# Kernel tuning notes

Hardware: AMD Instinct MI355X
Metric: run time of the kernel (lower is better)

Reference implementation:

```python
import jax
jax.config.update("jax_enable_x64", True)
import jax.numpy as jnp
import numpy as np

SAMPLE_RATE = 44100
HOP = 512
B, N_MELS, T = 8, 128, 2048
L = T * HOP  # 1,048,576 samples


def _lerp_up(x, out_len):
    # torch F.interpolate(mode='linear', align_corners=True): [B,C,Tin]->[B,C,out_len]
    t_in = x.shape[-1]
    pos = jnp.arange(out_len, dtype=jnp.float64) * ((t_in - 1) / (out_len - 1))
    i0 = jnp.floor(pos).astype(jnp.int32)
    i1 = jnp.minimum(i0 + 1, t_in - 1)
    w = (pos - i0).astype(x.dtype)
    return x[..., i0] * (1 - w) + x[..., i1] * w


def _conv1d(x, w, b, pad):
    y = jax.lax.conv_general_dilated(x, w, (1,), [(pad, pad)],
                                     dimension_numbers=("NCH", "OIH", "NCH"))
    return y + b[None, :, None]


def setup_inputs() -> dict:
    key = jax.random.key(0)
    ks = jax.random.split(key, 9)
    mel_frames = jax.random.normal(ks[0], (B, N_MELS, T), dtype=jnp.float32)
    # realistic f0: 80..380 Hz
    f0_frames = 80.0 + 300.0 * jax.random.uniform(ks[1], (B, T), dtype=jnp.float32)
    noise = jax.random.normal(ks[2], (B, L), dtype=jnp.float32)
    w1 = jax.random.normal(ks[3], (128, N_MELS, 7), dtype=jnp.float32) * 0.05
    b1 = jnp.zeros((128,), jnp.float32)
    w2 = jax.random.normal(ks[4], (128, 128, 3), dtype=jnp.float32) * 0.05
    b2 = jnp.zeros((128,), jnp.float32)
    w3 = jax.random.normal(ks[5], (2, 128, 3), dtype=jnp.float32) * 0.05
    b3 = jnp.zeros((2,), jnp.float32)
    return {"mel_frames": mel_frames, "f0_frames": f0_frames, "noise": noise,
            "w1": w1, "b1": b1, "w2": w2, "b2": b2, "w3": w3, "b3": b3}


def reference(mel_frames, f0_frames, noise, w1, b1, w2, b2, w3, b3):
    # --- comb source ---
    f0 = _lerp_up(f0_frames[:, None, :], L)  # [B,1,L]
    phase = jnp.cumsum(f0.astype(jnp.float64) / SAMPLE_RATE, axis=-1)
    phase = phase - jnp.round(phase)
    phase = phase.astype(f0.dtype)
    combtooth = jnp.sinc(SAMPLE_RATE * phase / (f0 + 1e-8))[:, 0, :]  # [B,L]
    # --- magnitude network ---
    h = jax.nn.leaky_relu(_conv1d(mel_frames, w1, b1, 3), 0.2)
    h = jax.nn.leaky_relu(_conv1d(h, w2, b2, 1), 0.2)
    mags = jnp.clip(_conv1d(h, w3, b3, 1), 0.0, 1.0)  # [B,2,T]
    mags = _lerp_up(mags, L)  # [B,2,L]
    noise_sig = jnp.clip(noise * mags[:, 0, :], -1.0, 1.0)
    comb_sig = jnp.clip(combtooth * mags[:, 1, :], -1.0, 1.0)
    signal = jnp.clip(noise_sig + comb_sig, -1.0, 1.0)
    return (signal[:, None, :], (comb_sig[:, None, :], noise_sig[:, None, :]))
```

## Files before the change

kernel.cpp:

```cpp
#include <hip/hip_runtime.h>
#include <math.h>

#define BATCH 8
#define NMEL 128
#define TT 2048
#define LL 1048576
#define NCHUNK 256
#define CHUNK 4096

static constexpr double RATIO  = 2047.0 / 1048575.0;
static constexpr float  RATIOF = (float)(2047.0 / 1048575.0);
static constexpr double INV_SR = 1.0 / 44100.0;

__global__ __launch_bounds__(256) void wtrans_kernel(
    const float* __restrict__ w1, const float* __restrict__ w2,
    float* __restrict__ w1t, float* __restrict__ w2t)
{
    int i = blockIdx.x * 256 + threadIdx.x;
    if (i < 896 * 128) {
        int m = i >> 7, co = i & 127;
        w1t[i] = w1[co * 896 + m];
    }
    if (i < 384 * 128) {
        int m = i >> 7, co = i & 127;
        w2t[i] = w2[co * 384 + m];
    }
}

#define XSTR 48
#define HSTR 44
__global__ __launch_bounds__(256, 3) void conv_chunk_kernel(
    const float* __restrict__ mel,
    const float* __restrict__ w1t,
    const float* __restrict__ b1,
    const float* __restrict__ w2t,
    const float* __restrict__ b2,
    const float* __restrict__ w3,
    const float* __restrict__ b3,
    float* __restrict__ mags,
    const float* __restrict__ f0f,
    double* __restrict__ sums)
{
    __shared__ __align__(16) float smem[NMEL * XSTR + NMEL * HSTR];
    int tid = threadIdx.x;
    int lane = tid & 63, wid = tid >> 6;

    if (blockIdx.x >= 512) {
        int cb = blockIdx.x - 512;
        int b = cb >> 8;
        int c = cb & (NCHUNK - 1);
        const float* row = f0f + b * TT;
        int start = c * CHUNK + tid * 16;
        double pos0 = (double)start * RATIO;
        int i0s = (int)pos0;
        float wb = (float)(pos0 - (double)i0s);
        int ib = i0s + 1 > TT - 1 ? TT - 1 : i0s + 1;
        int ic = i0s + 2 > TT - 1 ? TT - 1 : i0s + 2;
        float f0a = row[i0s], f0b = row[ib], f0c = row[ic];
        double s = 0.0;
        #pragma unroll
        for (int i = 0; i < 16; ++i) {
            float wi = wb + (float)i * RATIOF;
            bool hi = wi >= 1.0f;
            float w = hi ? wi - 1.0f : wi;
            float xa = hi ? f0b : f0a, xb = hi ? f0c : f0b;
            float f0 = xa * (1.0f - w) + xb * w;
            s += (double)f0 * INV_SR;
        }
        #pragma unroll
        for (int off = 32; off > 0; off >>= 1) s += __shfl_down(s, (unsigned)off, 64);
        double* dred = (double*)smem;
        if (lane == 0) dred[wid] = s;
        __syncthreads();
        if (tid == 0) sums[cb] = dred[0] + dred[1] + dred[2] + dred[3];
        return;
    }

    float* Xs  = smem;
    float* H1  = smem + NMEL * XSTR;
    float* H2  = smem;
    float* red = smem + NMEL * XSTR;

    int b  = blockIdx.x >> 6;
    int t0 = (blockIdx.x & 63) * 32;
    const float* melb = mel + (size_t)b * NMEL * TT;

    #pragma unroll
    for (int it = 0; it < 6; ++it) {
        int idx = tid + it * 256;
        int ci = idx / 12, q = idx - ci * 12;
        int t = t0 - 8 + q * 4;
        float4 v = make_float4(0.f, 0.f, 0.f, 0.f);
        if (t >= 0 && t + 3 < TT) v = *(const float4*)(melb + ci * TT + t);
        *(float4*)(&Xs[ci * XSTR + q * 4]) = v;
    }
    if (tid < 128) { H1[tid * HSTR + 0] = 0.f; H1[tid * HSTR + 41] = 0.f; }
    __syncthreads();

    int cog = tid >> 3;
    int tg  = tid & 7;
    int xbase = 1 + tg * 5;

    {
        float acc[4][5];
        #pragma unroll
        for (int j = 0; j < 4; ++j) {
            float bj = b1[cog * 4 + j];
            #pragma unroll
            for (int i = 0; i < 5; ++i) acc[j][i] = bj;
        }
        #pragma unroll 2
        for (int ci = 0; ci < NMEL; ++ci) {
            float xv[11];
            #pragma unroll
            for (int i = 0; i < 11; ++i) xv[i] = Xs[ci * XSTR + xbase + i];
            const float* wr = w1t + (size_t)(ci * 7) * 128 + cog * 4;
            #pragma unroll
            for (int k = 0; k < 7; ++k) {
                float4 w4 = *(const float4*)(wr + k * 128);
                float wv[4] = {w4.x, w4.y, w4.z, w4.w};
                #pragma unroll
                for (int j = 0; j < 4; ++j)
                    #pragma unroll
                    for (int i = 0; i < 5; ++i)
                        acc[j][i] = fmaf(wv[j], xv[i + k], acc[j][i]);
            }
        }
        #pragma unroll
        for (int j = 0; j < 4; ++j)
            #pragma unroll
            for (int i = 0; i < 5; ++i) {
                int t = t0 - 4 + tg * 5 + i;
                float v = acc[j][i];
                v = v > 0.0f ? v : 0.2f * v;
                if (t < 0 || t >= TT) v = 0.0f;
                H1[(cog * 4 + j) * HSTR + 1 + tg * 5 + i] = v;
            }
    }
    __syncthreads();

    {
        float acc[4][5];
        #pragma unroll
        for (int j = 0; j < 4; ++j) {
            float bj = b2[cog * 4 + j];
            #pragma unroll
            for (int i = 0; i < 5; ++i) acc[j][i] = bj;
        }
        int hbase = tg * 5;
        #pragma unroll 2
        for (int ci = 0; ci < NMEL; ++ci) {
            float xv[7];
            #pragma unroll
            for (int i = 0; i < 7; ++i) xv[i] = H1[ci * HSTR + hbase + i];
            const float* wr = w2t + (size_t)(ci * 3) * 128 + cog * 4;
            #pragma unroll
            for (int k = 0; k < 3; ++k) {
                float4 w4 = *(const float4*)(wr + k * 128);
                float wv[4] = {w4.x, w4.y, w4.z, w4.w};
                #pragma unroll
                for (int j = 0; j < 4; ++j)
                    #pragma unroll
                    for (int i = 0; i < 5; ++i)
                        acc[j][i] = fmaf(wv[j], xv[i + k], acc[j][i]);
            }
        }
        #pragma unroll
        for (int j = 0; j < 4; ++j)
            #pragma unroll
            for (int i = 0; i < 5; ++i) {
                int t = t0 - 4 + tg * 5 + i;
                float v = acc[j][i];
                v = v > 0.0f ? v : 0.2f * v;
                if (t < 0 || t >= TT) v = 0.0f;
                H2[(cog * 4 + j) * HSTR + tg * 5 + i] = v;
            }
    }
    __syncthreads();

    {
        int o   = tid >> 7;
        int cig = (tid >> 5) & 3;
        int tt  = tid & 31;
        float a = 0.0f;
        for (int cl = 0; cl < 32; ++cl) {
            int ci = cig * 32 + cl;
            #pragma unroll
            for (int k = 0; k < 3; ++k)
                a = fmaf(w3[o * 384 + ci * 3 + k], H2[ci * HSTR + tt + 3 + k], a);
        }
        red[(o * 4 + cig) * 32 + tt] = a;
    }
    __syncthreads();
    if (tid < 64) {
        int o = tid >> 5, tt = tid & 31;
        float s = b3[o] + red[(o * 4 + 0) * 32 + tt] + red[(o * 4 + 1) * 32 + tt]
                        + red[(o * 4 + 2) * 32 + tt] + red[(o * 4 + 3) * 32 + tt];
        s = fminf(fmaxf(s, 0.0f), 1.0f);
        mags[((size_t)b * 2 + o) * TT + t0 + tt] = s;
    }
}

__global__ __launch_bounds__(256, 4) void finalA_kernel(
    const float* __restrict__ f0f,
    const double* __restrict__ sums,
    float* __restrict__ fracs)
{
    int b = blockIdx.x >> 8;
    int c = blockIdx.x & (NCHUNK - 1);
    const float* row = f0f + b * TT;
    int tid = threadIdx.x;
    int lane = tid & 63, wid = tid >> 6;
    __shared__ double wsumP[4], wsumA[4];

    int chunkBase = c * CHUNK;
    int start = chunkBase + tid * 16;

    double part = (tid < c) ? sums[b * NCHUNK + tid] : 0.0;
    #pragma unroll
    for (int off = 32; off > 0; off >>= 1) part += __shfl_down(part, (unsigned)off, 64);
    if (lane == 0) wsumP[wid] = part;

    double pos0 = (double)start * RATIO;
    int i0s = (int)pos0;
    float wb = (float)(pos0 - (double)i0s);
    int ibk = i0s + 1 > TT - 1 ? TT - 1 : i0s + 1;
    int ick = i0s + 2 > TT - 1 ? TT - 1 : i0s + 2;
    float f0a = row[i0s], f0b = row[ibk], f0c = row[ick];
    float f0v[16];
    double s = 0.0;
    #pragma unroll
    for (int i = 0; i < 16; ++i) {
        float wi = wb + (float)i * RATIOF;
        bool hi = wi >= 1.0f;
        float w = hi ? wi - 1.0f : wi;
        float xa = hi ? f0b : f0a, xb = hi ? f0c : f0b;
        f0v[i] = xa * (1.0f - w) + xb * w;
        s += (double)f0v[i] * INV_SR;
    }
    double incl = s;
    #pragma unroll
    for (int off = 1; off < 64; off <<= 1) {
        double v = __shfl_up(incl, (unsigned)off, 64);
        if (lane >= off) incl += v;
    }
    if (lane == 63) wsumA[wid] = incl;
    __syncthreads();
    double run = wsumP[0] + wsumP[1] + wsumP[2] + wsumP[3] + (incl - s);
    for (int w = 0; w < wid; ++w) run += wsumA[w];

    float* fg = fracs + (size_t)b * LL + start;
    float fb4[4];
    #pragma unroll
    for (int i = 0; i < 16; ++i) {
        run += (double)f0v[i] * INV_SR;
        double fr = run - rint(run);
        fb4[i & 3] = (float)fr;
        if ((i & 3) == 3)
            *(float4*)(fg + (i & ~3)) = make_float4(fb4[0], fb4[1], fb4[2], fb4[3]);
    }
}

__global__ __launch_bounds__(256, 4) void finalB_kernel(
    const float* __restrict__ f0f,
    const float* __restrict__ noise,
    const float* __restrict__ mags,
    const float* __restrict__ fracs,
    float* __restrict__ out)
{
    int b = blockIdx.x >> 8;
    int c = blockIdx.x & (NCHUNK - 1);
    const float* row = f0f + b * TT;
    int tid = threadIdx.x;
    int chunkBase = c * CHUNK;

    const size_t BL = (size_t)BATCH * LL;
    const size_t outBase = (size_t)b * LL;
    const float* m0row = mags + (size_t)b * 2 * TT;
    const float* m1row = m0row + TT;

    #pragma unroll
    for (int g = 0; g < 4; ++g) {
        int G = g * 256 + tid;
        int n0 = chunkBase + G * 4;
        float4 fr4 = *(const float4*)(fracs + outBase + n0);
        const float* frp = (const float*)&fr4;
        float4 nz4 = *(const float4*)(noise + outBase + n0);
        const float* nzp = (const float*)&nz4;

        double posg = (double)n0 * RATIO;
        int i0a = (int)posg;
        float wf = (float)(posg - (double)i0a);
        int ib = i0a + 1 > TT - 1 ? TT - 1 : i0a + 1;
        int ic = i0a + 2 > TT - 1 ? TT - 1 : i0a + 2;
        float g0a = row[i0a],   g0b = row[ib],   g0c = row[ic];
        float m0a = m0row[i0a], m0b = m0row[ib], m0c = m0row[ic];
        float m1a = m1row[i0a], m1b = m1row[ib], m1c = m1row[ic];

        float so[4], co_[4], no_[4];
        #pragma unroll
        for (int j = 0; j < 4; ++j) {
            float wj = wf + (float)j * RATIOF;
            bool hi = wj >= 1.0f;
            float w = hi ? wj - 1.0f : wj;
            float xa = hi ? g0b : g0a, xb = hi ? g0c : g0b;
            float f0 = xa * (1.0f - w) + xb * w;
            float ya = hi ? m0b : m0a, yb = hi ? m0c : m0b;
            float m0 = ya * (1.0f - w) + yb * w;
            float za = hi ? m1b : m1a, zb = hi ? m1c : m1b;
            float m1 = za * (1.0f - w) + zb * w;

            float ph = frp[j];
            float x  = 44100.0f * ph * __builtin_amdgcn_rcpf(f0 + 1e-8f);
            float px = 3.14159265358979323f * x;
            float rr = 0.5f * x;
            float rf = rr - rintf(rr);
            float sn;
            asm("v_sin_f32 %0, %1" : "=v"(sn) : "v"(rf));
            float comb = (x == 0.0f) ? 1.0f : sn * __builtin_amdgcn_rcpf(px);

            float ns = fminf(fmaxf(nzp[j] * m0, -1.0f), 1.0f);
            float cs = fminf(fmaxf(comb * m1, -1.0f), 1.0f);
            so[j] = fminf(fmaxf(ns + cs, -1.0f), 1.0f);
            co_[j] = cs; no_[j] = ns;
        }
        *(float4*)(out + outBase + n0)          = make_float4(so[0], so[1], so[2], so[3]);
        *(float4*)(out + BL + outBase + n0)     = make_float4(co_[0], co_[1], co_[2], co_[3]);
        *(float4*)(out + 2 * BL + outBase + n0) = make_float4(no_[0], no_[1], no_[2], no_[3]);
    }
}

extern "C" void kernel_launch(void* const* d_in, const int* in_sizes, int n_in,
                              void* d_out, int out_size, void* d_ws, size_t ws_size,
                              hipStream_t stream) {
    const float* mel   = (const float*)d_in[0];
    const float* f0f   = (const float*)d_in[1];
    const float* noise = (const float*)d_in[2];
    const float* w1    = (const float*)d_in[3];
    const float* b1    = (const float*)d_in[4];
    const float* w2    = (const float*)d_in[5];
    const float* b2    = (const float*)d_in[6];
    const float* w3    = (const float*)d_in[7];
    const float* b3    = (const float*)d_in[8];
    float* out = (float*)d_out;

    float* w1t  = (float*)d_ws;
    float* w2t  = w1t + 896 * 128;
    float* mags = w2t + 384 * 128;
    double* sums = (double*)(mags + BATCH * 2 * TT);
    float* fracs = (float*)(sums + BATCH * NCHUNK);

    wtrans_kernel<<<(896 * 128 + 255) / 256, 256, 0, stream>>>(w1, w2, w1t, w2t);
    conv_chunk_kernel<<<512 + BATCH * NCHUNK, 256, 0, stream>>>(
        mel, w1t, b1, w2t, b2, w3, b3, mags, f0f, sums);
    finalA_kernel<<<BATCH * NCHUNK, 256, 0, stream>>>(f0f, sums, fracs);
    finalB_kernel<<<BATCH * NCHUNK, 256, 0, stream>>>(f0f, noise, mags, fracs, out);
}
```

Before: 265.8 us.

## Fuse phase scan with output stage and shrink conv tiles for more blocks

The two final kernels are merged so the per-sample phase fractions stay in swizzled shared memory instead of making a global round trip through a workspace buffer. The conv kernel now processes 16 time steps per block instead of 32, doubling the block count, cutting LDS use and raising the occupancy hint. The weight transpose uses a shared-memory tiled transpose so both reads and writes are coalesced. Smaller conv tiles recompute more halo columns, and the fused final kernel holds more registers and LDS per block.

```diff
diff --git a/kernel.cpp b/kernel.cpp
--- a/kernel.cpp
+++ b/kernel.cpp
@@ -16,20 +16,25 @@
     const float* __restrict__ w1, const float* __restrict__ w2,
     float* __restrict__ w1t, float* __restrict__ w2t)
 {
-    int i = blockIdx.x * 256 + threadIdx.x;
-    if (i < 896 * 128) {
-        int m = i >> 7, co = i & 127;
-        w1t[i] = w1[co * 896 + m];
-    }
-    if (i < 384 * 128) {
-        int m = i >> 7, co = i & 127;
-        w2t[i] = w2[co * 384 + m];
-    }
+    __shared__ float tile[32][33];
+    int blk = blockIdx.x;
+    const float* src; float* dst; int M, co0, m0;
+    if (blk < 112) { src = w1; dst = w1t; M = 896; co0 = (blk / 28) * 32; m0 = (blk % 28) * 32; }
+    else { blk -= 112; src = w2; dst = w2t; M = 384; co0 = (blk / 12) * 32; m0 = (blk % 12) * 32; }
+    int tx = threadIdx.x & 31, ty = threadIdx.x >> 5;
+    #pragma unroll
+    for (int r = 0; r < 4; ++r)
+        tile[ty + r * 8][tx] = src[(size_t)(co0 + ty + r * 8) * M + m0 + tx];
+    __syncthreads();
+    #pragma unroll
+    for (int r = 0; r < 4; ++r)
+        dst[(size_t)(m0 + ty + r * 8) * 128 + co0 + tx] = tile[tx][ty + r * 8];
 }
 
-#define XSTR 48
-#define HSTR 44
-__global__ __launch_bounds__(256, 3) void conv_chunk_kernel(
+#define XSTR 32
+#define H1STR 25
+#define H2STR 21
+__global__ __launch_bounds__(256, 5) void conv_chunk_kernel(
     const float* __restrict__ mel,
     const float* __restrict__ w1t,
     const float* __restrict__ b1,
@@ -41,12 +46,12 @@
     const float* __restrict__ f0f,
     double* __restrict__ sums)
 {
-    __shared__ __align__(16) float smem[NMEL * XSTR + NMEL * HSTR];
+    __shared__ __align__(16) float smem[NMEL * XSTR + NMEL * H1STR];
     int tid = threadIdx.x;
     int lane = tid & 63, wid = tid >> 6;
 
-    if (blockIdx.x >= 512) {
-        int cb = blockIdx.x - 512;
+    if (blockIdx.x >= 1024) {
+        int cb = blockIdx.x - 1024;
         int b = cb >> 8;
         int c = cb & (NCHUNK - 1);
         const float* row = f0f + b * TT;
@@ -81,39 +86,37 @@
     float* H2  = smem;
     float* red = smem + NMEL * XSTR;
 
-    int b  = blockIdx.x >> 6;
-    int t0 = (blockIdx.x & 63) * 32;
+    int b  = blockIdx.x >> 7;
+    int t0 = (blockIdx.x & 127) * 16;
     const float* melb = mel + (size_t)b * NMEL * TT;
 
     #pragma unroll
-    for (int it = 0; it < 6; ++it) {
+    for (int it = 0; it < 4; ++it) {
         int idx = tid + it * 256;
-        int ci = idx / 12, q = idx - ci * 12;
+        int ci = idx >> 3, q = idx & 7;
         int t = t0 - 8 + q * 4;
         float4 v = make_float4(0.f, 0.f, 0.f, 0.f);
         if (t >= 0 && t + 3 < TT) v = *(const float4*)(melb + ci * TT + t);
         *(float4*)(&Xs[ci * XSTR + q * 4]) = v;
     }
-    if (tid < 128) { H1[tid * HSTR + 0] = 0.f; H1[tid * HSTR + 41] = 0.f; }
-    __syncthreads();
-
-    int cog = tid >> 3;
-    int tg  = tid & 7;
-    int xbase = 1 + tg * 5;
+    __syncthreads();
 
     {
-        float acc[4][5];
+        int cog = tid >> 3;
+        int tg  = tid & 7;
+        int xbase = tg * 3 + 1;
+        float acc[4][3];
         #pragma unroll
         for (int j = 0; j < 4; ++j) {
             float bj = b1[cog * 4 + j];
             #pragma unroll
-            for (int i = 0; i < 5; ++i) acc[j][i] = bj;
+            for (int i = 0; i < 3; ++i) acc[j][i] = bj;
         }
         #pragma unroll 2
         for (int ci = 0; ci < NMEL; ++ci) {
-            float xv[11];
-            #pragma unroll
-            for (int i = 0; i < 11; ++i) xv[i] = Xs[ci * XSTR + xbase + i];
+            float xv[9];
+            #pragma unroll
+            for (int i = 0; i < 9; ++i) xv[i] = Xs[ci * XSTR + xbase + i];
             const float* wr = w1t + (size_t)(ci * 7) * 128 + cog * 4;
             #pragma unroll
             for (int k = 0; k < 7; ++k) {
@@ -122,95 +125,106 @@
                 #pragma unroll
                 for (int j = 0; j < 4; ++j)
                     #pragma unroll
-                    for (int i = 0; i < 5; ++i)
+                    for (int i = 0; i < 3; ++i)
                         acc[j][i] = fmaf(wv[j], xv[i + k], acc[j][i]);
             }
         }
         #pragma unroll
         for (int j = 0; j < 4; ++j)
             #pragma unroll
-            for (int i = 0; i < 5; ++i) {
-                int t = t0 - 4 + tg * 5 + i;
+            for (int i = 0; i < 3; ++i) {
+                int c1 = tg * 3 + i;
+                int t = t0 - 4 + c1;
                 float v = acc[j][i];
                 v = v > 0.0f ? v : 0.2f * v;
                 if (t < 0 || t >= TT) v = 0.0f;
-                H1[(cog * 4 + j) * HSTR + 1 + tg * 5 + i] = v;
+                H1[(cog * 4 + j) * H1STR + c1] = v;
             }
     }
     __syncthreads();
 
     {
-        float acc[4][5];
-        #pragma unroll
-        for (int j = 0; j < 4; ++j) {
-            float bj = b2[cog * 4 + j];
+        int cpg = tid >> 2;
+        int tg2 = tid & 3;
+        int hbase = tg2 * 5 + 1;
+        float acc[2][5];
+        #pragma unroll
+        for (int j = 0; j < 2; ++j) {
+            float bj = b2[cpg * 2 + j];
             #pragma unroll
             for (int i = 0; i < 5; ++i) acc[j][i] = bj;
         }
-        int hbase = tg * 5;
         #pragma unroll 2
         for (int ci = 0; ci < NMEL; ++ci) {
             float xv[7];
             #pragma unroll
-            for (int i = 0; i < 7; ++i) xv[i] = H1[ci * HSTR + hbase + i];
-            const float* wr = w2t + (size_t)(ci * 3) * 128 + cog * 4;
+            for (int i = 0; i < 7; ++i) xv[i] = H1[ci * H1STR + hbase + i];
+            const float* wr = w2t + (size_t)(ci * 3) * 128 + cpg * 2;
             #pragma unroll
             for (int k = 0; k < 3; ++k) {
-                float4 w4 = *(const float4*)(wr + k * 128);
-                float wv[4] = {w4.x, w4.y, w4.z, w4.w};
+                float2 w2v = *(const float2*)(wr + k * 128);
                 #pragma unroll
-                for (int j = 0; j < 4; ++j)
-                    #pragma unroll
-                    for (int i = 0; i < 5; ++i)
-                        acc[j][i] = fmaf(wv[j], xv[i + k], acc[j][i]);
+                for (int i = 0; i < 5; ++i) {
+                    acc[0][i] = fmaf(w2v.x, xv[i + k], acc[0][i]);
+                    acc[1][i] = fmaf(w2v.y, xv[i + k], acc[1][i]);
+                }
             }
         }
-        #pragma unroll
-        for (int j = 0; j < 4; ++j)
+        __syncthreads();
+        #pragma unroll
+        for (int j = 0; j < 2; ++j)
             #pragma unroll
             for (int i = 0; i < 5; ++i) {
-                int t = t0 - 4 + tg * 5 + i;
+                int c2 = tg2 * 5 + i;
+                int t = t0 - 2 + c2;
                 float v = acc[j][i];
                 v = v > 0.0f ? v : 0.2f * v;
                 if (t < 0 || t >= TT) v = 0.0f;
-                H2[(cog * 4 + j) * HSTR + tg * 5 + i] = v;
+                H2[(cpg * 2 + j) * H2STR + c2] = v;
             }
     }
     __syncthreads();
 
     {
         int o   = tid >> 7;
-        int cig = (tid >> 5) & 3;
-        int tt  = tid & 31;
+        int cig = (tid >> 4) & 7;
+        int tt  = tid & 15;
         float a = 0.0f;
-        for (int cl = 0; cl < 32; ++cl) {
-            int ci = cig * 32 + cl;
+        #pragma unroll 2
+        for (int cl = 0; cl < 16; ++cl) {
+            int ci = cig * 16 + cl;
             #pragma unroll
             for (int k = 0; k < 3; ++k)
-                a = fmaf(w3[o * 384 + ci * 3 + k], H2[ci * HSTR + tt + 3 + k], a);
-        }
-        red[(o * 4 + cig) * 32 + tt] = a;
-    }
-    __syncthreads();
-    if (tid < 64) {
-        int o = tid >> 5, tt = tid & 31;
-        float s = b3[o] + red[(o * 4 + 0) * 32 + tt] + red[(o * 4 + 1) * 32 + tt]
-                        + red[(o * 4 + 2) * 32 + tt] + red[(o * 4 + 3) * 32 + tt];
+                a = fmaf(w3[o * 384 + ci * 3 + k], H2[ci * H2STR + tt + 1 + k], a);
+        }
+        red[(o * 8 + cig) * 16 + tt] = a;
+    }
+    __syncthreads();
+    if (tid < 32) {
+        int o = tid >> 4, tt = tid & 15;
+        float s = b3[o];
+        #pragma unroll
+        for (int g = 0; g < 8; ++g) s += red[(o * 8 + g) * 16 + tt];
         s = fminf(fmaxf(s, 0.0f), 1.0f);
         mags[((size_t)b * 2 + o) * TT + t0 + tt] = s;
     }
 }
 
-__global__ __launch_bounds__(256, 4) void finalA_kernel(
+__device__ __forceinline__ int swz4(int g) { return g ^ ((g >> 3) & 7); }
+
+__global__ __launch_bounds__(256, 4) void final_kernel(
     const float* __restrict__ f0f,
+    const float* __restrict__ noise,
+    const float* __restrict__ mags,
     const double* __restrict__ sums,
-    float* __restrict__ fracs)
+    float* __restrict__ out)
 {
     int b = blockIdx.x >> 8;
     int c = blockIdx.x & (NCHUNK - 1);
     const float* row = f0f + b * TT;
     int tid = threadIdx.x;
     int lane = tid & 63, wid = tid >> 6;
+    __shared__ float4 fracsV[CHUNK / 4];
     __shared__ double wsumP[4], wsumA[4];
 
     int chunkBase = c * CHUNK;
@@ -249,7 +263,6 @@
     double run = wsumP[0] + wsumP[1] + wsumP[2] + wsumP[3] + (incl - s);
     for (int w = 0; w < wid; ++w) run += wsumA[w];
 
-    float* fg = fracs + (size_t)b * LL + start;
     float fb4[4];
     #pragma unroll
     for (int i = 0; i < 16; ++i) {
@@ -257,22 +270,9 @@
         double fr = run - rint(run);
         fb4[i & 3] = (float)fr;
         if ((i & 3) == 3)
-            *(float4*)(fg + (i & ~3)) = make_float4(fb4[0], fb4[1], fb4[2], fb4[3]);
-    }
-}
-
-__global__ __launch_bounds__(256, 4) void finalB_kernel(
-    const float* __restrict__ f0f,
-    const float* __restrict__ noise,
-    const float* __restrict__ mags,
-    const float* __restrict__ fracs,
-    float* __restrict__ out)
-{
-    int b = blockIdx.x >> 8;
-    int c = blockIdx.x & (NCHUNK - 1);
-    const float* row = f0f + b * TT;
-    int tid = threadIdx.x;
-    int chunkBase = c * CHUNK;
+            fracsV[swz4(tid * 4 + (i >> 2))] = make_float4(fb4[0], fb4[1], fb4[2], fb4[3]);
+    }
+    __syncthreads();
 
     const size_t BL = (size_t)BATCH * LL;
     const size_t outBase = (size_t)b * LL;
@@ -283,7 +283,7 @@
     for (int g = 0; g < 4; ++g) {
         int G = g * 256 + tid;
         int n0 = chunkBase + G * 4;
-        float4 fr4 = *(const float4*)(fracs + outBase + n0);
+        float4 fr4 = fracsV[swz4(G)];
         const float* frp = (const float*)&fr4;
         float4 nz4 = *(const float4*)(noise + outBase + n0);
         const float* nzp = (const float*)&nz4;
@@ -348,11 +348,9 @@
     float* w2t  = w1t + 896 * 128;
     float* mags = w2t + 384 * 128;
     double* sums = (double*)(mags + BATCH * 2 * TT);
-    float* fracs = (float*)(sums + BATCH * NCHUNK);
-
-    wtrans_kernel<<<(896 * 128 + 255) / 256, 256, 0, stream>>>(w1, w2, w1t, w2t);
-    conv_chunk_kernel<<<512 + BATCH * NCHUNK, 256, 0, stream>>>(
+
+    wtrans_kernel<<<160, 256, 0, stream>>>(w1, w2, w1t, w2t);
+    conv_chunk_kernel<<<1024 + BATCH * NCHUNK, 256, 0, stream>>>(
         mel, w1t, b1, w2t, b2, w3, b3, mags, f0f, sums);
-    finalA_kernel<<<BATCH * NCHUNK, 256, 0, stream>>>(f0f, sums, fracs);
-    finalB_kernel<<<BATCH * NCHUNK, 256, 0, stream>>>(f0f, noise, mags, fracs, out);
+    final_kernel<<<BATCH * NCHUNK, 256, 0, stream>>>(f0f, noise, mags, sums, out);
 }
```

New measurement: 304.0 us. 14.4% more time.

## Fuse phase scan with output stage via LDS, tile weight transpose, split conv launch

Applied to the files above, without the earlier changes.

The two final kernels are merged so the per-sample wrapped phase fractions stay in swizzled shared memory instead of making a round trip through a global scratch buffer. That removes a full write and read of an 8×1M float array. The weight transpose now uses a 32x32 shared-memory tile so both its reads and writes are coalesced. The conv/chunk-sum kernel is split into two launches of four batches each, which adds a launch but changes how the work is scheduled. The fused kernel uses more LDS per block, which may lower occupancy.

```diff
diff --git a/kernel.cpp b/kernel.cpp
--- a/kernel.cpp
+++ b/kernel.cpp
@@ -16,15 +16,19 @@
     const float* __restrict__ w1, const float* __restrict__ w2,
     float* __restrict__ w1t, float* __restrict__ w2t)
 {
-    int i = blockIdx.x * 256 + threadIdx.x;
-    if (i < 896 * 128) {
-        int m = i >> 7, co = i & 127;
-        w1t[i] = w1[co * 896 + m];
-    }
-    if (i < 384 * 128) {
-        int m = i >> 7, co = i & 127;
-        w2t[i] = w2[co * 384 + m];
-    }
+    __shared__ float tile[32][33];
+    int blk = blockIdx.x;
+    const float* src; float* dst; int M, co0, m0;
+    if (blk < 112) { src = w1; dst = w1t; M = 896; co0 = (blk / 28) * 32; m0 = (blk % 28) * 32; }
+    else { blk -= 112; src = w2; dst = w2t; M = 384; co0 = (blk / 12) * 32; m0 = (blk % 12) * 32; }
+    int tx = threadIdx.x & 31, ty = threadIdx.x >> 5;
+    #pragma unroll
+    for (int r = 0; r < 4; ++r)
+        tile[ty + r * 8][tx] = src[(size_t)(co0 + ty + r * 8) * M + m0 + tx];
+    __syncthreads();
+    #pragma unroll
+    for (int r = 0; r < 4; ++r)
+        dst[(size_t)(m0 + ty + r * 8) * 128 + co0 + tx] = tile[tx][ty + r * 8];
 }
 
 #define XSTR 48
@@ -39,15 +43,16 @@
     const float* __restrict__ b3,
     float* __restrict__ mags,
     const float* __restrict__ f0f,
-    double* __restrict__ sums)
+    double* __restrict__ sums,
+    int bbase)
 {
     __shared__ __align__(16) float smem[NMEL * XSTR + NMEL * HSTR];
     int tid = threadIdx.x;
     int lane = tid & 63, wid = tid >> 6;
 
-    if (blockIdx.x >= 512) {
-        int cb = blockIdx.x - 512;
-        int b = cb >> 8;
+    if (blockIdx.x >= 256) {
+        int cb = blockIdx.x - 256;
+        int b = bbase + (cb >> 8);
         int c = cb & (NCHUNK - 1);
         const float* row = f0f + b * TT;
         int start = c * CHUNK + tid * 16;
@@ -72,7 +77,7 @@
         double* dred = (double*)smem;
         if (lane == 0) dred[wid] = s;
         __syncthreads();
-        if (tid == 0) sums[cb] = dred[0] + dred[1] + dred[2] + dred[3];
+        if (tid == 0) sums[b * NCHUNK + c] = dred[0] + dred[1] + dred[2] + dred[3];
         return;
     }
 
@@ -81,7 +86,7 @@
     float* H2  = smem;
     float* red = smem + NMEL * XSTR;
 
-    int b  = blockIdx.x >> 6;
+    int b  = bbase + (blockIdx.x >> 6);
     int t0 = (blockIdx.x & 63) * 32;
     const float* melb = mel + (size_t)b * NMEL * TT;
 
@@ -201,16 +206,21 @@
     }
 }
 
-__global__ __launch_bounds__(256, 4) void finalA_kernel(
+__device__ __forceinline__ int swz4(int g) { return g ^ ((g >> 3) & 7); }
+
+__global__ __launch_bounds__(256, 4) void final_kernel(
     const float* __restrict__ f0f,
+    const float* __restrict__ noise,
+    const float* __restrict__ mags,
     const double* __restrict__ sums,
-    float* __restrict__ fracs)
+    float* __restrict__ out)
 {
     int b = blockIdx.x >> 8;
     int c = blockIdx.x & (NCHUNK - 1);
     const float* row = f0f + b * TT;
     int tid = threadIdx.x;
     int lane = tid & 63, wid = tid >> 6;
+    __shared__ float4 fracsV[CHUNK / 4];
     __shared__ double wsumP[4], wsumA[4];
 
     int chunkBase = c * CHUNK;
@@ -249,7 +259,6 @@
     double run = wsumP[0] + wsumP[1] + wsumP[2] + wsumP[3] + (incl - s);
     for (int w = 0; w < wid; ++w) run += wsumA[w];
 
-    float* fg = fracs + (size_t)b * LL + start;
     float fb4[4];
     #pragma unroll
     for (int i = 0; i < 16; ++i) {
@@ -257,22 +266,9 @@
         double fr = run - rint(run);
         fb4[i & 3] = (float)fr;
         if ((i & 3) == 3)
-            *(float4*)(fg + (i & ~3)) = make_float4(fb4[0], fb4[1], fb4[2], fb4[3]);
-    }
-}
-
-__global__ __launch_bounds__(256, 4) void finalB_kernel(
-    const float* __restrict__ f0f,
-    const float* __restrict__ noise,
-    const float* __restrict__ mags,
-    const float* __restrict__ fracs,
-    float* __restrict__ out)
-{
-    int b = blockIdx.x >> 8;
-    int c = blockIdx.x & (NCHUNK - 1);
-    const float* row = f0f + b * TT;
-    int tid = threadIdx.x;
-    int chunkBase = c * CHUNK;
+            fracsV[swz4(tid * 4 + (i >> 2))] = make_float4(fb4[0], fb4[1], fb4[2], fb4[3]);
+    }
+    __syncthreads();
 
     const size_t BL = (size_t)BATCH * LL;
     const size_t outBase = (size_t)b * LL;
@@ -283,7 +279,7 @@
     for (int g = 0; g < 4; ++g) {
         int G = g * 256 + tid;
         int n0 = chunkBase + G * 4;
-        float4 fr4 = *(const float4*)(fracs + outBase + n0);
+        float4 fr4 = fracsV[swz4(G)];
         const float* frp = (const float*)&fr4;
         float4 nz4 = *(const float4*)(noise + outBase + n0);
         const float* nzp = (const float*)&nz4;
@@ -348,11 +344,11 @@
     float* w2t  = w1t + 896 * 128;
     float* mags = w2t + 384 * 128;
     double* sums = (double*)(mags + BATCH * 2 * TT);
-    float* fracs = (float*)(sums + BATCH * NCHUNK);
-
-    wtrans_kernel<<<(896 * 128 + 255) / 256, 256, 0, stream>>>(w1, w2, w1t, w2t);
-    conv_chunk_kernel<<<512 + BATCH * NCHUNK, 256, 0, stream>>>(
-        mel, w1t, b1, w2t, b2, w3, b3, mags, f0f, sums);
-    finalA_kernel<<<BATCH * NCHUNK, 256, 0, stream>>>(f0f, sums, fracs);
-    finalB_kernel<<<BATCH * NCHUNK, 256, 0, stream>>>(f0f, noise, mags, fracs, out);
+
+    wtrans_kernel<<<160, 256, 0, stream>>>(w1, w2, w1t, w2t);
+    conv_chunk_kernel<<<256 + 4 * NCHUNK, 256, 0, stream>>>(
+        mel, w1t, b1, w2t, b2, w3, b3, mags, f0f, sums, 0);
+    conv_chunk_kernel<<<256 + 4 * NCHUNK, 256, 0, stream>>>(
+        mel, w1t, b1, w2t, b2, w3, b3, mags, f0f, sums, 4);
+    final_kernel<<<BATCH * NCHUNK, 256, 0, stream>>>(f0f, noise, mags, sums, out);
 }
```

Result: slower. 289.0 us (+8.7%).
